# Performance work log

Measured on AMD Instinct MI355X. Metric: run time of the kernel, lower is better.

Reference implementation:

```python
import jax, jax.numpy as jnp
import numpy as np

B, T, D, H = 4096, 200, 64, 64


def setup_inputs() -> dict:
    key = jax.random.key(0)
    k1, k2, k3, k4, k5 = jax.random.split(key, 5)
    rnn_input = jax.random.normal(k1, (B, T, D), dtype=jnp.float32)
    sequence_length = jax.random.randint(k2, (B, 1), 0, T, dtype=jnp.int32)
    att_score = jax.random.uniform(k3, (B, T, 1), dtype=jnp.float32)
    s = 1.0 / np.sqrt(D + H)
    W_gate = jax.random.uniform(k4, (D + H, 2 * H), dtype=jnp.float32, minval=-s, maxval=s)
    b_gate = jnp.ones((2 * H,), dtype=jnp.float32)  # TF GRUCell gate bias init = 1.0
    W_cand = jax.random.uniform(k5, (D + H, H), dtype=jnp.float32, minval=-s, maxval=s)
    b_cand = jnp.zeros((H,), dtype=jnp.float32)
    return {"rnn_input": rnn_input, "sequence_length": sequence_length,
            "att_score": att_score, "W_gate": W_gate, "b_gate": b_gate,
            "W_cand": W_cand, "b_cand": b_cand}


def _augru_scan(x, att, seq_len, W_gate, b_gate, W_cand, b_cand):
    # x: [B,T,D], att: [B,T,1], seq_len: [B]
    Bx, Tx, _ = x.shape
    Hx = W_cand.shape[1]
    xs = jnp.swapaxes(x, 0, 1)          # [T,B,D]
    ats = jnp.swapaxes(att, 0, 1)       # [T,B,1]
    mask = (jnp.arange(Tx)[:, None] < seq_len[None, :])[..., None]  # [T,B,1]

    def step(h, inp):
        x_t, a_t, m_t = inp
        ru = jax.nn.sigmoid(jnp.concatenate([x_t, h], axis=-1) @ W_gate + b_gate)
        r, u = ru[:, :Hx], ru[:, Hx:]
        c = jnp.tanh(jnp.concatenate([x_t, r * h], axis=-1) @ W_cand + b_cand)
        u = (1.0 - a_t) * u                      # VecAttGRUCell (AUGRU) gate modulation
        new_h = u * h + (1.0 - u) * c            # TF GRUCell convention
        out = jnp.where(m_t, new_h, 0.0)         # dynamic_rnn zeros outputs past seq_len
        h_next = jnp.where(m_t, new_h, h)        # state copied through past seq_len
        return h_next, out

    h0 = jnp.zeros((Bx, Hx), dtype=x.dtype)
    h_final, outs = jax.lax.scan(step, h0, (xs, ats, mask))
    return jnp.swapaxes(outs, 0, 1), h_final     # [B,T,H], [B,H]


def reference(rnn_input, sequence_length, att_score, W_gate, b_gate, W_cand, b_cand):
    seq_len = jnp.squeeze(sequence_length, axis=-1)
    rnn_output, _ = _augru_scan(rnn_input, att_score, seq_len,
                                W_gate, b_gate, W_cand, b_cand)
    return rnn_output  # return_sequence=True
```

## Files before the change

kernel.cpp:

```cpp
#include <hip/hip_runtime.h>


typedef _Float16 half4_t __attribute__((ext_vector_type(4)));
typedef _Float16 half8_t __attribute__((ext_vector_type(8)));
typedef float    f32x4  __attribute__((ext_vector_type(4)));

#define T_MAX 200
#define H_DIM 64
#define M_TILE 16

__device__ __forceinline__ f32x4 mfma16(half8_t a, half8_t b, f32x4 c) {
    return __builtin_amdgcn_mfma_f32_16x16x32_f16(a, b, c, 0, 0, 0);
}

__device__ __forceinline__ int swz(int row, int byteInRow) {
    return (row * 128 + byteInRow) ^ ((row & 7) << 4);
}

__global__ __launch_bounds__(256, 1) void augru_mfma(
    const float* __restrict__ X,
    const int*   __restrict__ SL,
    const float* __restrict__ ATT,
    const float* __restrict__ WG,
    const float* __restrict__ BG,
    const float* __restrict__ WC,
    const float* __restrict__ BC,
    float*       __restrict__ OUT)
{
    const int tid = threadIdx.x;
    const int w   = tid >> 6;
    const int l   = tid & 63;
    const int lr  = l & 15;
    const int lg  = l >> 4;
    const int b0  = blockIdx.x * M_TILE;

    __shared__ float     att_s[M_TILE][T_MAX];
    __shared__ int       sl_s[M_TILE];
    __shared__ _Float16  xb[2][M_TILE * 64];
    __shared__ _Float16  hb[M_TILE * 64];
    __shared__ _Float16  rhb[M_TILE * 64];
    __shared__ float     ub[M_TILE][65];

#pragma unroll
    for (int k = 0; k < 4; ++k) {
        int r = 4 * w + k;
        const float* ap = ATT + (size_t)(b0 + r) * T_MAX;
        for (int c = l; c < T_MAX; c += 64) att_s[r][c] = ap[c];
    }
    if (tid < M_TILE) {
        int v = SL[b0 + tid];
        sl_s[tid] = v < 0 ? 0 : (v > T_MAX ? T_MAX : v);
    }
    for (int i = tid; i < M_TILE * 64; i += 256) hb[i] = (_Float16)0.0f;
    {
        int r = tid >> 4, q = tid & 15;
        float4 v = *(const float4*)(X + ((size_t)(b0 + r) * T_MAX) * 64 + 4 * q);
        half4_t h4 = { (_Float16)v.x, (_Float16)v.y, (_Float16)v.z, (_Float16)v.w };
        *(half4_t*)((char*)xb[0] + swz(r, q * 8)) = h4;
    }

    half8_t wg[2][4];
    half8_t wc[4];
    float   bias_g[2], bias_c;
#pragma unroll
    for (int n = 0; n < 2; ++n) {
        int col = 16 * (2 * w + n) + lr;
#pragma unroll
        for (int kt = 0; kt < 4; ++kt) {
            int kbase = 32 * kt + 8 * lg;
            half8_t f;
#pragma unroll
            for (int j = 0; j < 8; ++j) f[j] = (_Float16)WG[(size_t)(kbase + j) * 128 + col];
            wg[n][kt] = f;
        }
        bias_g[n] = BG[col];
    }
    {
        int col = 16 * w + lr;
#pragma unroll
        for (int kt = 0; kt < 4; ++kt) {
            int kbase = 32 * kt + 8 * lg;
            half8_t f;
#pragma unroll
            for (int j = 0; j < 8; ++j) f[j] = (_Float16)WC[(size_t)(kbase + j) * 64 + col];
            wc[kt] = f;
        }
        bias_c = BC[col];
    }

    __syncthreads();

    int Lmax = 0;
#pragma unroll
    for (int r = 0; r < M_TILE; ++r) Lmax = max(Lmax, sl_s[r]);
    int Lrow[4];
#pragma unroll
    for (int k = 0; k < 4; ++k) Lrow[k] = sl_s[4 * lg + k];

    float hown[4] = {0.f, 0.f, 0.f, 0.f};
    const int ccol = 16 * w + lr;

    for (int t = 0; t < Lmax; ++t) {
        const int pb = t & 1;

        int tn = t + 1; if (tn > T_MAX - 1) tn = T_MAX - 1;
        const int xr = tid >> 4, xq = tid & 15;
        float4 xv = *(const float4*)(X + ((size_t)(b0 + xr) * T_MAX + tn) * 64 + 4 * xq);

        char* xbase = (char*)xb[pb];
        half8_t ax0 = *(half8_t*)(xbase + swz(lr, lg * 16));
        half8_t ax1 = *(half8_t*)(xbase + swz(lr, 64 + lg * 16));
        half8_t ah0 = *(half8_t*)((char*)hb + swz(lr, lg * 16));
        half8_t ah1 = *(half8_t*)((char*)hb + swz(lr, 64 + lg * 16));

        f32x4 accg[2];
#pragma unroll
        for (int n = 0; n < 2; ++n) {
            f32x4 acc = { bias_g[n], bias_g[n], bias_g[n], bias_g[n] };
            acc = mfma16(ax0, wg[n][0], acc);
            acc = mfma16(ax1, wg[n][1], acc);
            acc = mfma16(ah0, wg[n][2], acc);
            acc = mfma16(ah1, wg[n][3], acc);
            accg[n] = acc;
        }

        if (w < 2) {
#pragma unroll
            for (int n = 0; n < 2; ++n) {
                int col = 16 * (2 * w + n) + lr;
#pragma unroll
                for (int reg = 0; reg < 4; ++reg) {
                    int row = 4 * lg + reg;
                    float rr = __fdividef(1.f, 1.f + __expf(-accg[n][reg]));
                    float hv = (float)(*(_Float16*)((char*)hb + swz(row, col * 2)));
                    *(_Float16*)((char*)rhb + swz(row, col * 2)) = (_Float16)(rr * hv);
                }
            }
        } else {
#pragma unroll
            for (int reg = 0; reg < 4; ++reg) {
                int row = 4 * lg + reg;
                float a = att_s[row][t];
#pragma unroll
                for (int n = 0; n < 2; ++n) {
                    int ucol = 16 * (2 * (w - 2) + n) + lr;
                    float uu = __fdividef(1.f, 1.f + __expf(-accg[n][reg]));
                    ub[row][ucol] = (1.f - a) * uu;
                }
            }
        }
        __syncthreads();

        half8_t ar0 = *(half8_t*)((char*)rhb + swz(lr, lg * 16));
        half8_t ar1 = *(half8_t*)((char*)rhb + swz(lr, 64 + lg * 16));
        f32x4 accc = { bias_c, bias_c, bias_c, bias_c };
        accc = mfma16(ax0, wc[0], accc);
        accc = mfma16(ax1, wc[1], accc);
        accc = mfma16(ar0, wc[2], accc);
        accc = mfma16(ar1, wc[3], accc);

#pragma unroll
        for (int reg = 0; reg < 4; ++reg) {
            int row = 4 * lg + reg;
            float z  = accc[reg];
            float az = fabsf(z);
            float e2 = __expf(2.f * az);
            float c  = copysignf(1.f - __fdividef(2.f, e2 + 1.f), z);
            float uu = ub[row][ccol];
            float hn = uu * hown[reg] + (1.f - uu) * c;
            bool  m  = (t < Lrow[reg]);
            OUT[((size_t)(b0 + row) * T_MAX + t) * 64 + ccol] = m ? hn : 0.f;
            if (m) hown[reg] = hn;
            *(_Float16*)((char*)hb + swz(row, ccol * 2)) = (_Float16)hown[reg];
        }

        {
            half4_t h4 = { (_Float16)xv.x, (_Float16)xv.y, (_Float16)xv.z, (_Float16)xv.w };
            *(half4_t*)((char*)xb[pb ^ 1] + swz(xr, xq * 8)) = h4;
        }
        __syncthreads();
    }

    {
        uint4 z = make_uint4(0u, 0u, 0u, 0u);
#pragma unroll
        for (int k = 0; k < 4; ++k) {
            int r = 4 * w + k;
            uint4* zp = (uint4*)(OUT + ((size_t)(b0 + r) * T_MAX + Lmax) * 64);
            const int n4 = (T_MAX - Lmax) * (H_DIM / 4);
            for (int i = l; i < n4; i += 64) zp[i] = z;
        }
    }
}

extern "C" void kernel_launch(void* const* d_in, const int* in_sizes, int n_in,
                              void* d_out, int out_size, void* d_ws, size_t ws_size,
                              hipStream_t stream) {
    const float* X   = (const float*)d_in[0];
    const int*   SL  = (const int*)d_in[1];
    const float* ATT = (const float*)d_in[2];
    const float* WG  = (const float*)d_in[3];
    const float* BG  = (const float*)d_in[4];
    const float* WC  = (const float*)d_in[5];
    const float* BC  = (const float*)d_in[6];
    float*       OUT = (float*)d_out;

    const int B = in_sizes[1];
    dim3 grid(B / M_TILE), block(256);
    augru_mfma<<<grid, block, 0, stream>>>(X, SL, ATT, WG, BG, WC, BC, OUT);
}
```

Measured before the change: 503.9 us.

## Shrink batch tile to 4 rows per block for more blocks and occupancy

The tile drops from 16 to 4 batch rows per block, giving 1024 blocks instead of 256 and allowing up to 4 blocks per CU. Each wave now computes the r, u and candidate columns for its 16-column slice, so the shared u buffer and the role split between waves go away. The hidden state stays in registers of the lg==0 lanes, and x is prefetched two steps ahead using per-element loads. The cost is padded 16-row MFMAs that are three quarters empty, and only a quarter of the lanes doing the elementwise work.

```diff
diff --git a/kernel.cpp b/kernel.cpp
--- a/kernel.cpp
+++ b/kernel.cpp
@@ -1,23 +1,21 @@
 #include <hip/hip_runtime.h>
 
 
-typedef _Float16 half4_t __attribute__((ext_vector_type(4)));
 typedef _Float16 half8_t __attribute__((ext_vector_type(8)));
 typedef float    f32x4  __attribute__((ext_vector_type(4)));
 
 #define T_MAX 200
 #define H_DIM 64
-#define M_TILE 16
+#define M_TILE 4
 
 __device__ __forceinline__ f32x4 mfma16(half8_t a, half8_t b, f32x4 c) {
     return __builtin_amdgcn_mfma_f32_16x16x32_f16(a, b, c, 0, 0, 0);
 }
-
 __device__ __forceinline__ int swz(int row, int byteInRow) {
     return (row * 128 + byteInRow) ^ ((row & 7) << 4);
 }
 
-__global__ __launch_bounds__(256, 1) void augru_mfma(
+__global__ __launch_bounds__(256, 4) void augru_mfma(
     const float* __restrict__ X,
     const int*   __restrict__ SL,
     const float* __restrict__ ATT,
@@ -34,161 +32,131 @@
     const int lg  = l >> 4;
     const int b0  = blockIdx.x * M_TILE;
 
-    __shared__ float     att_s[M_TILE][T_MAX];
-    __shared__ int       sl_s[M_TILE];
-    __shared__ _Float16  xb[2][M_TILE * 64];
-    __shared__ _Float16  hb[M_TILE * 64];
-    __shared__ _Float16  rhb[M_TILE * 64];
-    __shared__ float     ub[M_TILE][65];
+    __shared__ float    att_s[M_TILE][T_MAX];
+    __shared__ int      sl_s[M_TILE];
+    __shared__ _Float16 xb[2][16 * 64];
+    __shared__ _Float16 hb[16 * 64];
+    __shared__ _Float16 rhb[16 * 64];
 
-#pragma unroll
-    for (int k = 0; k < 4; ++k) {
-        int r = 4 * w + k;
-        const float* ap = ATT + (size_t)(b0 + r) * T_MAX;
-        for (int c = l; c < T_MAX; c += 64) att_s[r][c] = ap[c];
+    for (int i = tid; i < 16 * 64; i += 256) {
+        xb[0][i] = (_Float16)0.f; xb[1][i] = (_Float16)0.f;
+        hb[i]    = (_Float16)0.f; rhb[i]   = (_Float16)0.f;
+    }
+    {
+        const float* ap = ATT + (size_t)(b0 + w) * T_MAX;
+        for (int c = l; c < T_MAX; c += 64) att_s[w][c] = ap[c];
     }
     if (tid < M_TILE) {
         int v = SL[b0 + tid];
         sl_s[tid] = v < 0 ? 0 : (v > T_MAX ? T_MAX : v);
     }
-    for (int i = tid; i < M_TILE * 64; i += 256) hb[i] = (_Float16)0.0f;
-    {
-        int r = tid >> 4, q = tid & 15;
-        float4 v = *(const float4*)(X + ((size_t)(b0 + r) * T_MAX) * 64 + 4 * q);
-        half4_t h4 = { (_Float16)v.x, (_Float16)v.y, (_Float16)v.z, (_Float16)v.w };
-        *(half4_t*)((char*)xb[0] + swz(r, q * 8)) = h4;
+
+    half8_t wgr[4], wgu[4], wcd[4];
+    const int cr = 16 * w + lr;
+    const int cu = 64 + cr;
+#pragma unroll
+    for (int kt = 0; kt < 4; ++kt) {
+        const int kb = 32 * kt + 8 * lg;
+        half8_t fr, fu, fc;
+#pragma unroll
+        for (int j = 0; j < 8; ++j) {
+            fr[j] = (_Float16)WG[(size_t)(kb + j) * 128 + cr];
+            fu[j] = (_Float16)WG[(size_t)(kb + j) * 128 + cu];
+            fc[j] = (_Float16)WC[(size_t)(kb + j) * 64 + cr];
+        }
+        wgr[kt] = fr; wgu[kt] = fu; wcd[kt] = fc;
     }
-
-    half8_t wg[2][4];
-    half8_t wc[4];
-    float   bias_g[2], bias_c;
-#pragma unroll
-    for (int n = 0; n < 2; ++n) {
-        int col = 16 * (2 * w + n) + lr;
-#pragma unroll
-        for (int kt = 0; kt < 4; ++kt) {
-            int kbase = 32 * kt + 8 * lg;
-            half8_t f;
-#pragma unroll
-            for (int j = 0; j < 8; ++j) f[j] = (_Float16)WG[(size_t)(kbase + j) * 128 + col];
-            wg[n][kt] = f;
-        }
-        bias_g[n] = BG[col];
-    }
-    {
-        int col = 16 * w + lr;
-#pragma unroll
-        for (int kt = 0; kt < 4; ++kt) {
-            int kbase = 32 * kt + 8 * lg;
-            half8_t f;
-#pragma unroll
-            for (int j = 0; j < 8; ++j) f[j] = (_Float16)WC[(size_t)(kbase + j) * 64 + col];
-            wc[kt] = f;
-        }
-        bias_c = BC[col];
-    }
+    const float bias_r = BG[cr], bias_u = BG[cu], bias_c = BC[cr];
 
     __syncthreads();
 
-    int Lmax = 0;
+    const float* xcol = X + ((size_t)(b0 + w) * T_MAX) * 64 + l;
+    const int a_stg = swz(w, 2 * l);
+    *(_Float16*)((char*)xb[0] + a_stg) = (_Float16)xcol[0];
+    float xv1 = xcol[64];
+
+    __syncthreads();
+
+    const int Lmax = max(max(sl_s[0], sl_s[1]), max(sl_s[2], sl_s[3]));
+    int Lrow[M_TILE];
 #pragma unroll
-    for (int r = 0; r < M_TILE; ++r) Lmax = max(Lmax, sl_s[r]);
-    int Lrow[4];
+    for (int r = 0; r < M_TILE; ++r) Lrow[r] = sl_s[r];
+
+    const int a_f0 = swz(lr, 16 * lg);
+    const int a_f1 = swz(lr, 64 + 16 * lg);
+    int a_c[M_TILE];
 #pragma unroll
-    for (int k = 0; k < 4; ++k) Lrow[k] = sl_s[4 * lg + k];
+    for (int r = 0; r < M_TILE; ++r) a_c[r] = swz(r, 2 * cr);
 
-    float hown[4] = {0.f, 0.f, 0.f, 0.f};
-    const int ccol = 16 * w + lr;
+    float hown[M_TILE] = {0.f, 0.f, 0.f, 0.f};
+    const size_t obase = (size_t)b0 * (T_MAX * H_DIM) + cr;
 
     for (int t = 0; t < Lmax; ++t) {
         const int pb = t & 1;
-
-        int tn = t + 1; if (tn > T_MAX - 1) tn = T_MAX - 1;
-        const int xr = tid >> 4, xq = tid & 15;
-        float4 xv = *(const float4*)(X + ((size_t)(b0 + xr) * T_MAX + tn) * 64 + 4 * xq);
+        int tn2 = t + 2; if (tn2 > T_MAX - 1) tn2 = T_MAX - 1;
+        float xv2 = xcol[(size_t)tn2 * 64];
 
         char* xbase = (char*)xb[pb];
-        half8_t ax0 = *(half8_t*)(xbase + swz(lr, lg * 16));
-        half8_t ax1 = *(half8_t*)(xbase + swz(lr, 64 + lg * 16));
-        half8_t ah0 = *(half8_t*)((char*)hb + swz(lr, lg * 16));
-        half8_t ah1 = *(half8_t*)((char*)hb + swz(lr, 64 + lg * 16));
+        half8_t ax0 = *(half8_t*)(xbase + a_f0);
+        half8_t ax1 = *(half8_t*)(xbase + a_f1);
+        half8_t ah0 = *(half8_t*)((char*)hb + a_f0);
+        half8_t ah1 = *(half8_t*)((char*)hb + a_f1);
 
-        f32x4 accg[2];
+        f32x4 accr = {bias_r, bias_r, bias_r, bias_r};
+        f32x4 accu = {bias_u, bias_u, bias_u, bias_u};
+        f32x4 accc = {bias_c, bias_c, bias_c, bias_c};
+        accr = mfma16(ax0, wgr[0], accr);  accu = mfma16(ax0, wgu[0], accu);
+        accc = mfma16(ax0, wcd[0], accc);
+        accr = mfma16(ax1, wgr[1], accr);  accu = mfma16(ax1, wgu[1], accu);
+        accc = mfma16(ax1, wcd[1], accc);
+        accr = mfma16(ah0, wgr[2], accr);  accu = mfma16(ah0, wgu[2], accu);
+        accr = mfma16(ah1, wgr[3], accr);  accu = mfma16(ah1, wgu[3], accu);
+
+        float uu[M_TILE];
+        if (lg == 0) {
 #pragma unroll
-        for (int n = 0; n < 2; ++n) {
-            f32x4 acc = { bias_g[n], bias_g[n], bias_g[n], bias_g[n] };
-            acc = mfma16(ax0, wg[n][0], acc);
-            acc = mfma16(ax1, wg[n][1], acc);
-            acc = mfma16(ah0, wg[n][2], acc);
-            acc = mfma16(ah1, wg[n][3], acc);
-            accg[n] = acc;
-        }
-
-        if (w < 2) {
-#pragma unroll
-            for (int n = 0; n < 2; ++n) {
-                int col = 16 * (2 * w + n) + lr;
-#pragma unroll
-                for (int reg = 0; reg < 4; ++reg) {
-                    int row = 4 * lg + reg;
-                    float rr = __fdividef(1.f, 1.f + __expf(-accg[n][reg]));
-                    float hv = (float)(*(_Float16*)((char*)hb + swz(row, col * 2)));
-                    *(_Float16*)((char*)rhb + swz(row, col * 2)) = (_Float16)(rr * hv);
-                }
-            }
-        } else {
-#pragma unroll
-            for (int reg = 0; reg < 4; ++reg) {
-                int row = 4 * lg + reg;
-                float a = att_s[row][t];
-#pragma unroll
-                for (int n = 0; n < 2; ++n) {
-                    int ucol = 16 * (2 * (w - 2) + n) + lr;
-                    float uu = __fdividef(1.f, 1.f + __expf(-accg[n][reg]));
-                    ub[row][ucol] = (1.f - a) * uu;
-                }
+            for (int r = 0; r < M_TILE; ++r) {
+                float rv = __fdividef(1.f, 1.f + __expf(-accr[r]));
+                *(_Float16*)((char*)rhb + a_c[r]) = (_Float16)(rv * hown[r]);
+                float a = att_s[r][t];
+                uu[r] = (1.f - a) * __fdividef(1.f, 1.f + __expf(-accu[r]));
             }
         }
         __syncthreads();
 
-        half8_t ar0 = *(half8_t*)((char*)rhb + swz(lr, lg * 16));
-        half8_t ar1 = *(half8_t*)((char*)rhb + swz(lr, 64 + lg * 16));
-        f32x4 accc = { bias_c, bias_c, bias_c, bias_c };
-        accc = mfma16(ax0, wc[0], accc);
-        accc = mfma16(ax1, wc[1], accc);
-        accc = mfma16(ar0, wc[2], accc);
-        accc = mfma16(ar1, wc[3], accc);
+        half8_t ar0 = *(half8_t*)((char*)rhb + a_f0);
+        half8_t ar1 = *(half8_t*)((char*)rhb + a_f1);
+        accc = mfma16(ar0, wcd[2], accc);
+        accc = mfma16(ar1, wcd[3], accc);
 
+        if (lg == 0) {
 #pragma unroll
-        for (int reg = 0; reg < 4; ++reg) {
-            int row = 4 * lg + reg;
-            float z  = accc[reg];
-            float az = fabsf(z);
-            float e2 = __expf(2.f * az);
-            float c  = copysignf(1.f - __fdividef(2.f, e2 + 1.f), z);
-            float uu = ub[row][ccol];
-            float hn = uu * hown[reg] + (1.f - uu) * c;
-            bool  m  = (t < Lrow[reg]);
-            OUT[((size_t)(b0 + row) * T_MAX + t) * 64 + ccol] = m ? hn : 0.f;
-            if (m) hown[reg] = hn;
-            *(_Float16*)((char*)hb + swz(row, ccol * 2)) = (_Float16)hown[reg];
+            for (int r = 0; r < M_TILE; ++r) {
+                float z  = accc[r];
+                float az = fabsf(z);
+                float e2 = __expf(2.f * az);
+                float c  = copysignf(1.f - __fdividef(2.f, e2 + 1.f), z);
+                float hn = uu[r] * hown[r] + (1.f - uu[r]) * c;
+                bool  m  = (t < Lrow[r]);
+                OUT[obase + (size_t)r * (T_MAX * H_DIM) + (size_t)t * H_DIM]
+                    = m ? hn : 0.f;
+                if (m) hown[r] = hn;
+                *(_Float16*)((char*)hb + a_c[r]) = (_Float16)hown[r];
+            }
         }
 
-        {
-            half4_t h4 = { (_Float16)xv.x, (_Float16)xv.y, (_Float16)xv.z, (_Float16)xv.w };
-            *(half4_t*)((char*)xb[pb ^ 1] + swz(xr, xq * 8)) = h4;
-        }
+        *(_Float16*)((char*)xb[pb ^ 1] + a_stg) = (_Float16)xv1;
+        xv1 = xv2;
         __syncthreads();
     }
 
     {
-        uint4 z = make_uint4(0u, 0u, 0u, 0u);
+        uint4 zz = make_uint4(0u, 0u, 0u, 0u);
+        const int n4 = (T_MAX - Lmax) * (H_DIM / 4);
 #pragma unroll
-        for (int k = 0; k < 4; ++k) {
-            int r = 4 * w + k;
-            uint4* zp = (uint4*)(OUT + ((size_t)(b0 + r) * T_MAX + Lmax) * 64);
-            const int n4 = (T_MAX - Lmax) * (H_DIM / 4);
-            for (int i = l; i < n4; i += 64) zp[i] = z;
+        for (int r = 0; r < M_TILE; ++r) {
+            uint4* zp = (uint4*)(OUT + ((size_t)(b0 + r) * T_MAX + Lmax) * H_DIM);
+            for (int i = tid; i < n4; i += 256) zp[i] = zz;
         }
     }
 }
```

New measurement: 683.6 us. 35.7% more time.
